# Kernel optimization log

Measured on AMD Instinct MI355X. Metric: run time of the kernel, lower is better.

The kernel has to match this reference:

```python
import jax, jax.numpy as jnp
import numpy as np

B, L, HS, WS = 4, 5, 32, 32
C = 256            # dim == heads * dim_head
M, D = 8, 32       # heads, dim_head
T, R = 2, 4        # num_types, num_relations
I = M * D          # inner_dim
EPS = 1e-5


def setup_inputs() -> dict:
    key = jax.random.key(0)
    ks = jax.random.split(key, 12)
    w = 0.02
    x = jax.random.normal(ks[0], (B, L, HS, WS, C), dtype=jnp.float32)
    mask = jnp.ones((B, HS, WS, L, L), dtype=jnp.int32)
    prior_encoding = jax.random.randint(ks[1], (B, L, HS, WS, 3), 0, T).astype(jnp.float32)
    return {
        "x": x,
        "mask": mask,
        "prior_encoding": prior_encoding,
        "ln_w": jnp.ones((C,), jnp.float32),
        "ln_b": jnp.zeros((C,), jnp.float32),
        "Wq": jax.random.normal(ks[2], (T, C, I), jnp.float32) * w,
        "bq": jnp.zeros((T, I), jnp.float32),
        "Wk": jax.random.normal(ks[3], (T, C, I), jnp.float32) * w,
        "bk": jnp.zeros((T, I), jnp.float32),
        "Wv": jax.random.normal(ks[4], (T, C, I), jnp.float32) * w,
        "bv": jnp.zeros((T, I), jnp.float32),
        "Wa": jax.random.normal(ks[5], (T, I, C), jnp.float32) * w,
        "ba": jnp.zeros((T, C), jnp.float32),
        "rel_att": jax.random.normal(ks[6], (R, M, D, D), jnp.float32) * w,
        "rel_msg": jax.random.normal(ks[7], (R, M, D, D), jnp.float32) * w,
    }


def _hgt_forward(x, mask, prior_encoding, ln_w, ln_b, Wq, bq, Wk, bk, Wv, bv, Wa, ba, rel_att, rel_msg):
    # pre-LayerNorm over channel dim
    mu = jnp.mean(x, axis=-1, keepdims=True)
    var = jnp.mean(jnp.square(x - mu), axis=-1, keepdims=True)
    xn = (x - mu) * jax.lax.rsqrt(var + EPS) * ln_w + ln_b

    # [B,L,H,W,C] -> [B,H,W,L,C]
    xp = jnp.transpose(xn, (0, 2, 3, 1, 4))
    types = prior_encoding[:, :, 0, 0, 2].astype(jnp.int32)  # [B,L]

    # per-type q/k/v projections via gather of type-indexed weights
    q = jnp.einsum('bhwlc,blci->bhwli', xp, Wq[types]) + bq[types][:, None, None]
    k = jnp.einsum('bhwlc,blci->bhwli', xp, Wk[types]) + bk[types][:, None, None]
    v = jnp.einsum('bhwlc,blci->bhwli', xp, Wv[types]) + bv[types][:, None, None]

    def to_heads(t):  # [B,H,W,L,I] -> [B,M,H,W,L,D]
        return jnp.transpose(t.reshape(B, HS, WS, L, M, D), (0, 4, 1, 2, 3, 5))
    q, k, v = to_heads(q), to_heads(k), to_heads(v)

    # relation-indexed edge weights: e_type = t_i * T + t_j
    e = types[:, :, None] * T + types[:, None, :]              # [B,L,L]
    w_att = jnp.transpose(rel_att[e], (0, 3, 1, 2, 4, 5))      # [B,M,L,L,D,D]
    w_msg = jnp.transpose(rel_msg[e], (0, 3, 1, 2, 4, 5))

    scale = D ** -0.5
    q_w = jnp.einsum('bmhwip,bmijpq->bmhwijq', q, w_att)
    att = jnp.einsum('bmhwijq,bmhwjq->bmhwij', q_w, k) * scale
    att = jnp.where(mask[:, None] == 0, -1e9, att)
    att = jax.nn.softmax(att, axis=-1)

    v_msg = jnp.einsum('bmijpc,bmhwjp->bmhwijc', w_msg, v)
    out = jnp.einsum('bmhwij,bmhwijc->bmhwic', att, v_msg)

    # [B,M,H,W,L,D] -> [B,H,W,L,C]
    out = jnp.transpose(out, (0, 2, 3, 4, 1, 5)).reshape(B, HS, WS, L, I)
    out = jnp.einsum('bhwli,blic->bhwlc', out, Wa[types]) + ba[types][:, None, None]
    # dropout is identity at inference
    return jnp.transpose(out, (0, 3, 1, 2, 4))                 # [B,L,H,W,C]


def reference(x, mask, prior_encoding, ln_w, ln_b, Wq, bq, Wk, bk, Wv, bv, Wa, ba, rel_att, rel_msg):
    return _hgt_forward(x, mask, prior_encoding, ln_w, ln_b, Wq, bq, Wk, bk, Wv, bv, Wa, ba, rel_att, rel_msg)
```

## Files before the change

kernel.cpp:

```cpp
#include <hip/hip_runtime.h>
#include <hip/hip_bf16.h>
#include <math.h>

#define BB 4
#define LL 5
#define HSZ 32
#define WSZ 32
#define PP (HSZ*WSZ)
#define CC 256
#define MM 8
#define DD 32
#define II 256
#define TT 2
#define NTOK (BB*PP*LL*II)
#define TILE_ELEMS 8192
#define SCALE 0.17677669529663687f

typedef short bf16x8 __attribute__((ext_vector_type(8)));
typedef float f32x4 __attribute__((ext_vector_type(4)));

static __device__ __forceinline__ ushort f2bf(float f) {
    unsigned u = __float_as_uint(f);
    unsigned r = (u + 0x7fffu + ((u >> 16) & 1u)) >> 16;
    return (ushort)r;
}
static __device__ __forceinline__ float bf2f(ushort u) {
    return __uint_as_float(((unsigned)u) << 16);
}

__global__ __launch_bounds__(256) void k_fold(
    const float* __restrict__ Wq, const float* __restrict__ Wv,
    const float* __restrict__ Wk, const float* __restrict__ Wa,
    const float* __restrict__ bq, const float* __restrict__ bv,
    const float* __restrict__ rel_att, const float* __restrict__ rel_msg,
    const float* __restrict__ x,
    const float* __restrict__ lnw, const float* __restrict__ lnb,
    ushort* __restrict__ packW, float* __restrict__ bEff,
    ushort* __restrict__ xnPack)
{
    __shared__ float As[1024];
    __shared__ ushort Apack[8192];
    const int blk = blockIdx.x;
    const int tid = threadIdx.x;

    if (blk < 64) {
        const int p  = blk >> 5;
        const int t  = (blk >> 4) & 1;
        const int ts = (blk >> 3) & 1;
        const int m  = blk & 7;
        const float* A = (p == 0)
            ? rel_att + (size_t)((t * 2 + ts) * 8 + m) * 1024
            : rel_msg + (size_t)((ts * 2 + t) * 8 + m) * 1024;
        for (int i = tid; i < 1024; i += 256) As[i] = A[i];
        __syncthreads();

        const float* W = ((p == 0) ? Wq : Wv) + (size_t)t * 65536;
        const int k = tid;
        float wrow[32];
        #pragma unroll
        for (int u = 0; u < 8; ++u)
            *(float4*)&wrow[u * 4] = *(const float4*)&W[k * 256 + m * 32 + u * 4];

        const int slot = (p == 0 ? 0 : 4) + t * 2 + ts;
        ushort* base = packW + (size_t)slot * 65536;
        const int kt = k >> 5, j = k & 7, lq = ((k >> 3) & 3) * 16;
        #pragma unroll
        for (int q = 0; q < 32; ++q) {
            float acc = 0.f;
            #pragma unroll
            for (int pp = 0; pp < 32; ++pp) acc += wrow[pp] * As[pp * 32 + q];
            const int nt = m * 2 + (q >> 4);
            const int lane = lq + (q & 15);
            base[(size_t)((nt * 8 + kt) * 64 + lane) * 8 + j] = f2bf(acc);
        }
        if (tid < 32) {
            const int q = tid;
            const float* bi = ((p == 0) ? bq : bv) + t * 256 + m * 32;
            float acc = 0.f;
            #pragma unroll
            for (int pp = 0; pp < 32; ++pp) acc += bi[pp] * As[pp * 32 + q];
            bEff[(p ? 1024 : 0) + (t * 2 + ts) * 256 + m * 32 + q] = acc;
        }
    } else if (blk < 192) {
        const int idx = blk - 64;
        const int which = idx >> 6;
        const int gi = (idx & 63) * 256 + tid;
        const int t = gi >> 13;
        const int sub = gi & 8191;
        const float* src = ((which == 0) ? Wk : Wa) + (size_t)t * 65536;
        const int slot = (which == 0 ? 8 : 10) + t;
        const int nt = sub >> 9, kt = (sub >> 6) & 7, lane = sub & 63;
        const int k0 = kt * 32 + (lane >> 4) * 8;
        const int n  = nt * 16 + (lane & 15);
        ushort h[8];
        #pragma unroll
        for (int j = 0; j < 8; ++j) h[j] = f2bf(src[(size_t)(k0 + j) * 256 + n]);
        uint4 o;
        o.x = (unsigned)h[0] | ((unsigned)h[1] << 16);
        o.y = (unsigned)h[2] | ((unsigned)h[3] << 16);
        o.z = (unsigned)h[4] | ((unsigned)h[5] << 16);
        o.w = (unsigned)h[6] | ((unsigned)h[7] << 16);
        *(uint4*)(packW + (size_t)slot * 65536 + (size_t)sub * 8) = o;
    } else {
        const int lblk = blk - 192;
        const int bl  = lblk >> 5;
        const int pt  = lblk & 31;
        const int p0  = pt * 32;

        const int r  = tid >> 3;
        const int jj = tid & 7;
        const float* xrow = x + ((size_t)bl * PP + p0 + r) * CC;
        float4 xv[8];
        float s1 = 0.f, s2 = 0.f;
        #pragma unroll
        for (int u = 0; u < 8; ++u) {
            xv[u] = *(const float4*)(xrow + jj * 32 + u * 4);
            s1 += xv[u].x + xv[u].y + xv[u].z + xv[u].w;
            s2 += xv[u].x * xv[u].x + xv[u].y * xv[u].y + xv[u].z * xv[u].z + xv[u].w * xv[u].w;
        }
        s1 += __shfl_xor(s1, 1); s1 += __shfl_xor(s1, 2); s1 += __shfl_xor(s1, 4);
        s2 += __shfl_xor(s2, 1); s2 += __shfl_xor(s2, 2); s2 += __shfl_xor(s2, 4);
        const float mu   = s1 * (1.0f / 256.0f);
        const float var  = s2 * (1.0f / 256.0f) - mu * mu;
        const float rstd = rsqrtf(var + 1e-5f);

        const int mt_r = r >> 4, rm = r & 15;
        #pragma unroll
        for (int u = 0; u < 8; ++u) {
            const int c0 = jj * 32 + u * 4;
            const float4 g  = *(const float4*)(lnw + c0);
            const float4 bt = *(const float4*)(lnb + c0);
            const ushort h0 = f2bf((xv[u].x - mu) * rstd * g.x + bt.x);
            const ushort h1 = f2bf((xv[u].y - mu) * rstd * g.y + bt.y);
            const ushort h2 = f2bf((xv[u].z - mu) * rstd * g.z + bt.z);
            const ushort h3 = f2bf((xv[u].w - mu) * rstd * g.w + bt.w);
            uint2 w2;
            w2.x = (unsigned)h0 | ((unsigned)h1 << 16);
            w2.y = (unsigned)h2 | ((unsigned)h3 << 16);
            const int kt   = c0 >> 5;
            const int lsub = rm + (((c0 >> 3) & 3) << 4);
            const int j0   = c0 & 7;
            *(uint2*)&Apack[(((mt_r * 8 + kt) * 64 + lsub) << 3) + j0] = w2;
        }
        __syncthreads();

        const size_t tbase = (size_t)lblk * TILE_ELEMS;
        #pragma unroll
        for (int u = 0; u < 4; ++u) {
            const int ch = (tid + u * 256) * 8;
            *(uint4*)&xnPack[tbase + ch] = *(const uint4*)&Apack[ch];
        }
    }
}

__global__ __launch_bounds__(256) void k_proj(
    const ushort* __restrict__ xnPack, const float* __restrict__ prior,
    const ushort* __restrict__ packW, const float* __restrict__ bEff,
    const float* __restrict__ bk,
    ushort* __restrict__ qw0, ushort* __restrict__ qw1, ushort* __restrict__ kkO,
    ushort* __restrict__ vm0, ushort* __restrict__ vm1)
{
    __shared__ ushort As[8192];

    const int tid  = threadIdx.x;
    const int blk  = blockIdx.x;
    const int mat  = blk / 640;
    const int rem  = blk - mat * 640;
    const int bl   = rem >> 5;
    const int sub  = rem & 31;
    const int pg   = sub >> 1;
    const int half = sub & 1;
    const int t    = (int)prior[(size_t)bl * (PP * 3) + 2];

    int slot; const float* bias;
    if (mat < 2)       { slot = t * 2 + mat;           bias = bEff + slot * 256; }
    else if (mat == 2) { slot = 8 + t;                 bias = bk + t * 256; }
    else               { slot = 4 + t * 2 + (mat - 3); bias = bEff + 1024 + (t * 2 + (mat - 3)) * 256; }
    ushort* dst = (mat == 0) ? qw0 : (mat == 1) ? qw1 : (mat == 2) ? kkO : (mat == 3) ? vm0 : vm1;

    const int wv = tid >> 6, lane = tid & 63;

    const ushort* Bp = packW + (size_t)slot * 65536;
    bf16x8 bfr[8][2];
    #pragma unroll
    for (int kt = 0; kt < 8; ++kt)
        #pragma unroll
        for (int nn = 0; nn < 2; ++nn) {
            const int ntg = half * 8 + wv * 2 + nn;
            bfr[kt][nn] = *(const bf16x8*)&Bp[(size_t)((ntg * 8 + kt) * 64 + lane) * 8];
        }

    const int cl = lane & 15, rq = lane >> 4;
    const int colA = half * 128 + wv * 32 + cl;
    const int colB = colA + 16;
    const float biasA = bias[colA], biasB = bias[colB];

    #pragma unroll 1
    for (int tl = 0; tl < 2; ++tl) {
        const int pt = pg * 2 + tl;
        const size_t tbase = (size_t)(bl * 32 + pt) * TILE_ELEMS;
        __syncthreads();
        #pragma unroll
        for (int u = 0; u < 4; ++u) {
            const int ch = (tid + u * 256) * 8;
            *(uint4*)&As[ch] = *(const uint4*)&xnPack[tbase + ch];
        }
        __syncthreads();

        f32x4 acc[2][2];
        #pragma unroll
        for (int mt = 0; mt < 2; ++mt)
            #pragma unroll
            for (int nn = 0; nn < 2; ++nn)
                acc[mt][nn] = (f32x4){0.f, 0.f, 0.f, 0.f};

        #pragma unroll
        for (int kt = 0; kt < 8; ++kt) {
            const bf16x8 a0 = *(const bf16x8*)&As[((0 * 8 + kt) * 64 + lane) << 3];
            const bf16x8 a1 = *(const bf16x8*)&As[((1 * 8 + kt) * 64 + lane) << 3];
            acc[0][0] = __builtin_amdgcn_mfma_f32_16x16x32_bf16(a0, bfr[kt][0], acc[0][0], 0, 0, 0);
            acc[0][1] = __builtin_amdgcn_mfma_f32_16x16x32_bf16(a0, bfr[kt][1], acc[0][1], 0, 0, 0);
            acc[1][0] = __builtin_amdgcn_mfma_f32_16x16x32_bf16(a1, bfr[kt][0], acc[1][0], 0, 0, 0);
            acc[1][1] = __builtin_amdgcn_mfma_f32_16x16x32_bf16(a1, bfr[kt][1], acc[1][1], 0, 0, 0);
        }

        const int p0 = pt * 32;
        #pragma unroll
        for (int mt = 0; mt < 2; ++mt) {
            const int row0 = p0 + mt * 16 + rq * 4;
            #pragma unroll
            for (int r2 = 0; r2 < 4; ++r2) {
                const size_t rb = ((size_t)bl * PP + row0 + r2) * II;
                dst[rb + colA] = f2bf(acc[mt][0][r2] + biasA);
                dst[rb + colB] = f2bf(acc[mt][1][r2] + biasB);
            }
        }
    }
}

__global__ __launch_bounds__(512) void k_attn_out(
    const ushort* __restrict__ qw0, const ushort* __restrict__ qw1,
    const ushort* __restrict__ kkI,
    const ushort* __restrict__ vm0, const ushort* __restrict__ vm1,
    const int* __restrict__ mask, const float* __restrict__ prior,
    const ushort* __restrict__ packW, const float* __restrict__ ba,
    float* __restrict__ out)
{
    __shared__ ushort aoS[5 * 8 * 264];
    __shared__ float obufF[8 * 260];

    const int tid  = threadIdx.x;
    const int blk  = blockIdx.x;
    const int b    = blk >> 7;
    const int pg   = blk & 127;
    const int p0   = pg * 8;
    const int wv   = tid >> 6, lane = tid & 63;
    const int c0   = lane * 4;

    int ty[5];
    #pragma unroll
    for (int l = 0; l < 5; ++l)
        ty[l] = (int)prior[(size_t)(b * 5 + l) * (PP * 3) + 2];

    {
        const int sl   = wv;
        const int pix  = p0 + sl;
        const int site = b * 1024 + pix;
        const int usite = __builtin_amdgcn_readfirstlane(site);

        ushort4 rq0[5], rq1[5], rkv[5], rv0[5], rv1[5];
        #pragma unroll
        for (int l = 0; l < 5; ++l) {
            const size_t base = (((size_t)(b * 5 + l) << 10) + pix) * II + c0;
            rq0[l] = *(const ushort4*)(qw0 + base);
            rq1[l] = *(const ushort4*)(qw1 + base);
            rkv[l] = *(const ushort4*)(kkI + base);
            rv0[l] = *(const ushort4*)(vm0 + base);
            rv1[l] = *(const ushort4*)(vm1 + base);
        }

        int mv[5][5];
        #pragma unroll
        for (int i = 0; i < 5; ++i)
            #pragma unroll
            for (int j = 0; j < 5; ++j)
                mv[i][j] = mask[(size_t)usite * 25 + i * 5 + j];

        float qf[2][5][4], kf[5][4];
        #pragma unroll
        for (int l = 0; l < 5; ++l) {
            qf[0][l][0] = bf2f(rq0[l].x); qf[0][l][1] = bf2f(rq0[l].y);
            qf[0][l][2] = bf2f(rq0[l].z); qf[0][l][3] = bf2f(rq0[l].w);
            qf[1][l][0] = bf2f(rq1[l].x); qf[1][l][1] = bf2f(rq1[l].y);
            qf[1][l][2] = bf2f(rq1[l].z); qf[1][l][3] = bf2f(rq1[l].w);
            kf[l][0]    = bf2f(rkv[l].x); kf[l][1]    = bf2f(rkv[l].y);
            kf[l][2]    = bf2f(rkv[l].z); kf[l][3]    = bf2f(rkv[l].w);
        }

        float s[5][5];
        #pragma unroll
        for (int j = 0; j < 5; ++j) {
            if (ty[j]) {
                #pragma unroll
                for (int i = 0; i < 5; ++i)
                    s[i][j] = qf[1][i][0] * kf[j][0] + qf[1][i][1] * kf[j][1]
                            + qf[1][i][2] * kf[j][2] + qf[1][i][3] * kf[j][3];
            } else {
                #pragma unroll
                for (int i = 0; i < 5; ++i)
                    s[i][j] = qf[0][i][0] * kf[j][0] + qf[0][i][1] * kf[j][1]
                            + qf[0][i][2] * kf[j][2] + qf[0][i][3] * kf[j][3];
            }
        }
        #pragma unroll
        for (int i = 0; i < 5; ++i)
            #pragma unroll
            for (int j = 0; j < 5; ++j) s[i][j] += __shfl_xor(s[i][j], 1);
        #pragma unroll
        for (int i = 0; i < 5; ++i)
            #pragma unroll
            for (int j = 0; j < 5; ++j) s[i][j] += __shfl_xor(s[i][j], 2);
        #pragma unroll
        for (int i = 0; i < 5; ++i)
            #pragma unroll
            for (int j = 0; j < 5; ++j) s[i][j] += __shfl_xor(s[i][j], 4);

        float vf[2][5][4];
        #pragma unroll
        for (int l = 0; l < 5; ++l) {
            vf[0][l][0] = bf2f(rv0[l].x); vf[0][l][1] = bf2f(rv0[l].y);
            vf[0][l][2] = bf2f(rv0[l].z); vf[0][l][3] = bf2f(rv0[l].w);
            vf[1][l][0] = bf2f(rv1[l].x); vf[1][l][1] = bf2f(rv1[l].y);
            vf[1][l][2] = bf2f(rv1[l].z); vf[1][l][3] = bf2f(rv1[l].w);
        }

        #pragma unroll
        for (int i = 0; i < 5; ++i) {
            float lg[5];
            #pragma unroll
            for (int j = 0; j < 5; ++j)
                lg[j] = mv[i][j] ? s[i][j] * SCALE : -1e9f;
            const float mx = fmaxf(fmaxf(fmaxf(lg[0], lg[1]), fmaxf(lg[2], lg[3])), lg[4]);
            float ex[5], sum = 0.f;
            #pragma unroll
            for (int j = 0; j < 5; ++j) { ex[j] = __expf(lg[j] - mx); sum += ex[j]; }
            const float rs = 1.0f / sum;
            float o0 = 0.f, o1 = 0.f, o2 = 0.f, o3 = 0.f;
            if (ty[i]) {
                #pragma unroll
                for (int j = 0; j < 5; ++j) {
                    o0 += ex[j] * vf[1][j][0]; o1 += ex[j] * vf[1][j][1];
                    o2 += ex[j] * vf[1][j][2]; o3 += ex[j] * vf[1][j][3];
                }
            } else {
                #pragma unroll
                for (int j = 0; j < 5; ++j) {
                    o0 += ex[j] * vf[0][j][0]; o1 += ex[j] * vf[0][j][1];
                    o2 += ex[j] * vf[0][j][2]; o3 += ex[j] * vf[0][j][3];
                }
            }
            o0 *= rs; o1 *= rs; o2 *= rs; o3 *= rs;
            uint2 w2;
            w2.x = (unsigned)f2bf(o0) | ((unsigned)f2bf(o1) << 16);
            w2.y = (unsigned)f2bf(o2) | ((unsigned)f2bf(o3) << 16);
            *(uint2*)&aoS[(i * 8 + sl) * 264 + c0] = w2;
        }
    }
    __syncthreads();

    const int half = wv >> 2;
    const int wv2  = wv & 3;
    const int cl = lane & 15, rq = lane >> 4;
    const int rowA8 = lane & 7;
    const int ksub = (lane >> 4) * 8;
    const int colL_A = wv2 * 32 + cl;
    const int colL_B = colL_A + 16;

    #pragma unroll 1
    for (int l = 0; l < 5; ++l) {
        const int t = ty[l];
        const ushort* Bp = packW + (size_t)(10 + t) * 65536;
        bf16x8 bfr[8][2];
        #pragma unroll
        for (int kt = 0; kt < 8; ++kt)
            #pragma unroll
            for (int nn = 0; nn < 2; ++nn) {
                const int ntg = half * 8 + wv2 * 2 + nn;
                bfr[kt][nn] = *(const bf16x8*)&Bp[(size_t)((ntg * 8 + kt) * 64 + lane) * 8];
            }

        f32x4 acc[2];
        acc[0] = (f32x4){0.f, 0.f, 0.f, 0.f};
        acc[1] = (f32x4){0.f, 0.f, 0.f, 0.f};

        const ushort* aRow = &aoS[(l * 8 + rowA8) * 264 + ksub];
        #pragma unroll
        for (int kt = 0; kt < 8; ++kt) {
            const bf16x8 a0 = *(const bf16x8*)(aRow + kt * 32);
            acc[0] = __builtin_amdgcn_mfma_f32_16x16x32_bf16(a0, bfr[kt][0], acc[0], 0, 0, 0);
            acc[1] = __builtin_amdgcn_mfma_f32_16x16x32_bf16(a0, bfr[kt][1], acc[1], 0, 0, 0);
        }

        const float biasA = ba[t * CC + half * 128 + colL_A];
        const float biasB = ba[t * CC + half * 128 + colL_B];

        __syncthreads();
        if (rq < 2) {
            #pragma unroll
            for (int r2 = 0; r2 < 4; ++r2) {
                obufF[(rq * 4 + r2) * 260 + half * 128 + colL_A] = acc[0][r2] + biasA;
                obufF[(rq * 4 + r2) * 260 + half * 128 + colL_B] = acc[1][r2] + biasB;
            }
        }
        __syncthreads();

        const int row = tid >> 6;
        const int ch  = (tid & 63) * 4;
        const float4 v4 = *(const float4*)&obufF[row * 260 + ch];
        *(float4*)(out + ((size_t)(b * LL + l) * PP + p0 + row) * CC + ch) = v4;
    }
}

extern "C" void kernel_launch(void* const* d_in, const int* in_sizes, int n_in,
                              void* d_out, int out_size, void* d_ws, size_t ws_size,
                              hipStream_t stream) {
    const float* x       = (const float*)d_in[0];
    const int*   mask    = (const int*)d_in[1];
    const float* prior   = (const float*)d_in[2];
    const float* lnw     = (const float*)d_in[3];
    const float* lnb     = (const float*)d_in[4];
    const float* Wq      = (const float*)d_in[5];
    const float* bq      = (const float*)d_in[6];
    const float* Wk      = (const float*)d_in[7];
    const float* bk      = (const float*)d_in[8];
    const float* Wv      = (const float*)d_in[9];
    const float* bv      = (const float*)d_in[10];
    const float* Wa      = (const float*)d_in[11];
    const float* ba      = (const float*)d_in[12];
    const float* rel_att = (const float*)d_in[13];
    const float* rel_msg = (const float*)d_in[14];
    float* out = (float*)d_out;

    ushort* qw0    = (ushort*)d_ws;
    ushort* qw1    = qw0 + NTOK;
    ushort* kko    = qw1 + NTOK;
    ushort* vm0    = kko + NTOK;
    ushort* vm1    = vm0 + NTOK;
    ushort* xnPack = vm1 + NTOK;
    ushort* packW  = xnPack + NTOK;
    float*  bEff   = (float*)(packW + 12 * 65536);

    hipLaunchKernelGGL(k_fold, dim3(832), dim3(256), 0, stream,
                       Wq, Wv, Wk, Wa, bq, bv, rel_att, rel_msg,
                       x, lnw, lnb, packW, bEff, xnPack);
    hipLaunchKernelGGL(k_proj, dim3(3200), dim3(256), 0, stream,
                       xnPack, prior, packW, bEff, bk, qw0, qw1, kko, vm0, vm1);
    hipLaunchKernelGGL(k_attn_out, dim3(512), dim3(512), 0, stream,
                       qw0, qw1, kko, vm0, vm1, mask, prior, packW, ba, out);
}
```

Before: 154.2 us.

## Process 16 pixels per block in attention-output kernel to fill MFMA rows

The attention/output kernel now handles 16 pixels per block with 1024 threads instead of 8 pixels with 512. Each wave computes one 16-column tile of the output projection using all 16 MFMA rows, instead of wasting half the rows on 8 valid pixels. Per-wave weight fragment loads are halved. The cost is fewer blocks (256) and larger blocks with more LDS and register pressure, which may lower occupancy.

```diff
diff --git a/kernel.cpp b/kernel.cpp
--- a/kernel.cpp
+++ b/kernel.cpp
@@ -238,7 +238,7 @@
     }
 }
 
-__global__ __launch_bounds__(512) void k_attn_out(
+__global__ __launch_bounds__(1024) void k_attn_out(
     const ushort* __restrict__ qw0, const ushort* __restrict__ qw1,
     const ushort* __restrict__ kkI,
     const ushort* __restrict__ vm0, const ushort* __restrict__ vm1,
@@ -246,14 +246,14 @@
     const ushort* __restrict__ packW, const float* __restrict__ ba,
     float* __restrict__ out)
 {
-    __shared__ ushort aoS[5 * 8 * 264];
-    __shared__ float obufF[8 * 260];
+    __shared__ ushort aoS[5 * 16 * 264];
+    __shared__ float obufF[16 * 260];
 
     const int tid  = threadIdx.x;
     const int blk  = blockIdx.x;
-    const int b    = blk >> 7;
-    const int pg   = blk & 127;
-    const int p0   = pg * 8;
+    const int b    = blk >> 6;
+    const int pg   = blk & 63;
+    const int p0   = pg * 16;
     const int wv   = tid >> 6, lane = tid & 63;
     const int c0   = lane * 4;
 
@@ -363,55 +363,40 @@
             uint2 w2;
             w2.x = (unsigned)f2bf(o0) | ((unsigned)f2bf(o1) << 16);
             w2.y = (unsigned)f2bf(o2) | ((unsigned)f2bf(o3) << 16);
-            *(uint2*)&aoS[(i * 8 + sl) * 264 + c0] = w2;
+            *(uint2*)&aoS[(i * 16 + sl) * 264 + c0] = w2;
         }
     }
     __syncthreads();
 
-    const int half = wv >> 2;
-    const int wv2  = wv & 3;
+    const int ntg  = wv;
     const int cl = lane & 15, rq = lane >> 4;
-    const int rowA8 = lane & 7;
-    const int ksub = (lane >> 4) * 8;
-    const int colL_A = wv2 * 32 + cl;
-    const int colL_B = colL_A + 16;
+    const int rowA = lane & 15;
+    const int ksub = rq * 8;
+    const int colG = ntg * 16 + cl;
 
     #pragma unroll 1
     for (int l = 0; l < 5; ++l) {
         const int t = ty[l];
         const ushort* Bp = packW + (size_t)(10 + t) * 65536;
-        bf16x8 bfr[8][2];
+        bf16x8 bfr[8];
         #pragma unroll
         for (int kt = 0; kt < 8; ++kt)
-            #pragma unroll
-            for (int nn = 0; nn < 2; ++nn) {
-                const int ntg = half * 8 + wv2 * 2 + nn;
-                bfr[kt][nn] = *(const bf16x8*)&Bp[(size_t)((ntg * 8 + kt) * 64 + lane) * 8];
-            }
-
-        f32x4 acc[2];
-        acc[0] = (f32x4){0.f, 0.f, 0.f, 0.f};
-        acc[1] = (f32x4){0.f, 0.f, 0.f, 0.f};
-
-        const ushort* aRow = &aoS[(l * 8 + rowA8) * 264 + ksub];
+            bfr[kt] = *(const bf16x8*)&Bp[(size_t)((ntg * 8 + kt) * 64 + lane) * 8];
+
+        f32x4 acc = (f32x4){0.f, 0.f, 0.f, 0.f};
+        const ushort* aRow = &aoS[(l * 16 + rowA) * 264 + ksub];
         #pragma unroll
         for (int kt = 0; kt < 8; ++kt) {
             const bf16x8 a0 = *(const bf16x8*)(aRow + kt * 32);
-            acc[0] = __builtin_amdgcn_mfma_f32_16x16x32_bf16(a0, bfr[kt][0], acc[0], 0, 0, 0);
-            acc[1] = __builtin_amdgcn_mfma_f32_16x16x32_bf16(a0, bfr[kt][1], acc[1], 0, 0, 0);
-        }
-
-        const float biasA = ba[t * CC + half * 128 + colL_A];
-        const float biasB = ba[t * CC + half * 128 + colL_B];
-
-        __syncthreads();
-        if (rq < 2) {
-            #pragma unroll
-            for (int r2 = 0; r2 < 4; ++r2) {
-                obufF[(rq * 4 + r2) * 260 + half * 128 + colL_A] = acc[0][r2] + biasA;
-                obufF[(rq * 4 + r2) * 260 + half * 128 + colL_B] = acc[1][r2] + biasB;
-            }
-        }
+            acc = __builtin_amdgcn_mfma_f32_16x16x32_bf16(a0, bfr[kt], acc, 0, 0, 0);
+        }
+
+        const float bias = ba[t * CC + colG];
+
+        __syncthreads();
+        #pragma unroll
+        for (int r2 = 0; r2 < 4; ++r2)
+            obufF[(rq * 4 + r2) * 260 + colG] = acc[r2] + bias;
         __syncthreads();
 
         const int row = tid >> 6;
@@ -455,6 +440,6 @@
                        x, lnw, lnb, packW, bEff, xnPack);
     hipLaunchKernelGGL(k_proj, dim3(3200), dim3(256), 0, stream,
                        xnPack, prior, packW, bEff, bk, qw0, qw1, kko, vm0, vm1);
-    hipLaunchKernelGGL(k_attn_out, dim3(512), dim3(512), 0, stream,
+    hipLaunchKernelGGL(k_attn_out, dim3(256), dim3(1024), 0, stream,
                        qw0, qw1, kko, vm0, vm1, mask, prior, packW, ba, out);
 }
```

Result: no change. 151.7 us (-1.6%).
